# Kernel optimization log

Hardware: AMD Instinct MI355X
Metric: run time of the kernel (lower is better)

Reference implementation:

```python
import jax, jax.numpy as jnp
import numpy as np

IN_DIM, OUT_DIM = 256, 128
N_NODES, N_EDGES = 50000, 800000


def _glorot(key, shape):
    fan_in = shape[-1]
    return jax.random.normal(key, shape, dtype=jnp.float32) / jnp.sqrt(jnp.float32(fan_in))


def setup_inputs() -> dict:
    key = jax.random.key(0)
    ks = jax.random.split(key, 16)
    features1 = jax.random.normal(ks[0], (N_NODES, IN_DIM), dtype=jnp.float32)
    edge_index = jax.random.randint(ks[1], (2, N_EDGES), 0, N_NODES, dtype=jnp.int32)
    return {
        "features1": features1,
        "edge_index": edge_index,
        # encoder conv1: in->out
        "Wl_e1": _glorot(ks[2], (OUT_DIM, IN_DIM)), "bl_e1": jnp.zeros((OUT_DIM,), jnp.float32), "Wr_e1": _glorot(ks[3], (OUT_DIM, IN_DIM)),
        # encoder conv2: out->out
        "Wl_e2": _glorot(ks[4], (OUT_DIM, OUT_DIM)), "bl_e2": jnp.zeros((OUT_DIM,), jnp.float32), "Wr_e2": _glorot(ks[5], (OUT_DIM, OUT_DIM)),
        # fc: out->out
        "W_fc": _glorot(ks[6], (OUT_DIM, OUT_DIM)), "b_fc": jnp.zeros((OUT_DIM,), jnp.float32),
        # decoder conv1: out->out
        "Wl_d1": _glorot(ks[7], (OUT_DIM, OUT_DIM)), "bl_d1": jnp.zeros((OUT_DIM,), jnp.float32), "Wr_d1": _glorot(ks[8], (OUT_DIM, OUT_DIM)),
        # decoder conv2: out->in
        "Wl_d2": _glorot(ks[9], (IN_DIM, OUT_DIM)), "bl_d2": jnp.zeros((IN_DIM,), jnp.float32), "Wr_d2": _glorot(ks[10], (IN_DIM, OUT_DIM)),
    }


def _sage_conv(x, src, dst, inv_deg, Wl, bl, Wr):
    # mean aggregation of neighbor messages x[src] at destination nodes
    agg = jax.ops.segment_sum(x[src], dst, num_segments=N_NODES) * inv_deg  # [N, d_in]
    out = agg @ Wl.T + bl + x @ Wr.T  # lin_l(agg) + lin_r(x)
    # F.normalize(out, p=2, dim=-1)
    nrm = jnp.maximum(jnp.linalg.norm(out, axis=-1, keepdims=True), 1e-12)
    return out / nrm


def reference(features1, edge_index, Wl_e1, bl_e1, Wr_e1, Wl_e2, bl_e2, Wr_e2,
              W_fc, b_fc, Wl_d1, bl_d1, Wr_d1, Wl_d2, bl_d2, Wr_d2):
    src, dst = edge_index[0], edge_index[1]
    deg = jax.ops.segment_sum(jnp.ones((src.shape[0],), jnp.float32), dst, num_segments=N_NODES)
    inv_deg = (1.0 / jnp.maximum(deg, 1.0))[:, None]
    # encoder
    h = _sage_conv(features1, src, dst, inv_deg, Wl_e1, bl_e1, Wr_e1)
    x1 = _sage_conv(h, src, dst, inv_deg, Wl_e2, bl_e2, Wr_e2)
    # bottleneck linear
    x = x1 @ W_fc.T + b_fc
    # decoder
    h = _sage_conv(x, src, dst, inv_deg, Wl_d1, bl_d1, Wr_d1)
    x1_rec = _sage_conv(h, src, dst, inv_deg, Wl_d2, bl_d2, Wr_d2)
    return (x1, x1_rec)
```

## Files before the change

### kernel.cpp

```cpp
#include <hip/hip_runtime.h>
#include <hip/hip_bf16.h>
#include <math.h>

#define N_NODES 50000
#define N_EDGES 800000
#define SLOT_CAP 64

typedef short s16x8 __attribute__((ext_vector_type(8)));
typedef float f32x4 __attribute__((ext_vector_type(4)));

static __device__ __forceinline__ unsigned short f2bf(float x) {
    __hip_bfloat16 b = __float2bfloat16(x);
    return *(unsigned short*)&b;
}
static __device__ __forceinline__ float2 bfu2f2(unsigned int u) {
    __hip_bfloat162 b = *(__hip_bfloat162*)&u;
    return __bfloat1622float2(b);
}
static __device__ __forceinline__ unsigned int packbf2(float x, float y) {
    return (unsigned int)f2bf(x) | ((unsigned int)f2bf(y) << 16);
}

__global__ void k_fillslot(const int* __restrict__ src, const int* __restrict__ dst,
                           int* __restrict__ cnt, unsigned short* __restrict__ slots) {
    int e = blockIdx.x * blockDim.x + threadIdx.x;
    if (e >= N_EDGES) return;
    int d = dst[e];
    int pos = atomicAdd(&cnt[d], 1);
    if (pos < SLOT_CAP) slots[d * SLOT_CAP + pos] = (unsigned short)src[e];
}

#define FEATN (N_NODES * 256)
#define O_WL_E1 (FEATN)
#define O_WR_E1 (FEATN + 32768)
#define O_WL_E2 (FEATN + 65536)
#define O_WR_E2 (FEATN + 81920)
#define O_W_FC  (FEATN + 98304)
#define O_WL_D1 (FEATN + 114688)
#define O_WR_D1 (FEATN + 131072)
#define O_D2    (FEATN + 147456)
#define PREP_TOT (FEATN + 212992)

__global__ __launch_bounds__(256) void k_prep(const float* __restrict__ feat,
                                              const float* __restrict__ wle1, const float* __restrict__ wre1,
                                              const float* __restrict__ wle2, const float* __restrict__ wre2,
                                              const float* __restrict__ wfc,
                                              const float* __restrict__ wld1, const float* __restrict__ wrd1,
                                              const float* __restrict__ wld2, const float* __restrict__ wrd2,
                                              unsigned short* __restrict__ dstp) {
    const int tot4 = PREP_TOT / 4;
    for (int i = blockIdx.x * blockDim.x + threadIdx.x; i < tot4; i += gridDim.x * blockDim.x) {
        int e = i * 4;
        const float* s;
        int off;
        if      (e < O_WL_E1) { s = feat; off = e; }
        else if (e < O_WR_E1) { s = wle1; off = e - O_WL_E1; }
        else if (e < O_WL_E2) { s = wre1; off = e - O_WR_E1; }
        else if (e < O_WR_E2) { s = wle2; off = e - O_WL_E2; }
        else if (e < O_W_FC)  { s = wre2; off = e - O_WR_E2; }
        else if (e < O_WL_D1) { s = wfc;  off = e - O_W_FC; }
        else if (e < O_WR_D1) { s = wld1; off = e - O_WL_D1; }
        else if (e < O_D2)    { s = wrd1; off = e - O_WR_D1; }
        else {
            int rel = e - O_D2;
            int row = rel >> 8, half = (rel >> 7) & 1, col = rel & 127;
            s = half ? wrd2 : wld2;
            off = row * 128 + col;
        }
        float4 v = *(const float4*)&s[off];
        ushort4 u;
        u.x = f2bf(v.x); u.y = f2bf(v.y); u.z = f2bf(v.z); u.w = f2bf(v.w);
        *(ushort4*)&dstp[e] = u;
    }
}

template <int K>
__global__ __launch_bounds__(256) void k_gmm2(const unsigned short* __restrict__ X,
                                              const unsigned short* __restrict__ W,
                                              const float* __restrict__ bias0,
                                              const float* __restrict__ bias1,
                                              unsigned short* __restrict__ Y,
                                              int N, int Ystride) {
    constexpr int CH = K / 8;
    __shared__ unsigned short Ws[128 * K];
    const unsigned short* Wsrc = W + (size_t)blockIdx.y * 128 * K;
    for (int idx = threadIdx.x; idx < 128 * CH; idx += 256) {
        int n = idx / CH, c = idx % CH;
        uint4 v = *(const uint4*)&Wsrc[n * K + c * 8];
        int cs = c ^ (n & 15);
        *(uint4*)&Ws[n * K + cs * 8] = v;
    }
    __syncthreads();

    const int wid = threadIdx.x >> 6, lane = threadIdx.x & 63;
    const int row0 = blockIdx.x * 128 + wid * 32;
    const int lrow = lane & 15;
    const int lk8  = lane >> 4;
    f32x4 acc[2][8] = {};

    s16x8 a_cur[2];
#pragma unroll
    for (int i = 0; i < 2; i++) {
        int r = row0 + i * 16 + lrow;
        s16x8 av = {};
        if (r < N) av = *(const s16x8*)&X[(size_t)r * K + lk8 * 8];
        a_cur[i] = av;
    }

#pragma unroll
    for (int ks = 0; ks < K; ks += 32) {
        s16x8 a_nxt[2] = {};
        if (ks + 32 < K) {
#pragma unroll
            for (int i = 0; i < 2; i++) {
                int r = row0 + i * 16 + lrow;
                if (r < N) a_nxt[i] = *(const s16x8*)&X[(size_t)r * K + ks + 32 + lk8 * 8];
            }
        }
#pragma unroll
        for (int nf = 0; nf < 8; nf++) {
            int n = nf * 16 + lrow;
            int c = (ks >> 3) + lk8;
            int cs = c ^ (n & 15);
            s16x8 b = *(const s16x8*)&Ws[n * K + cs * 8];
            acc[0][nf] = __builtin_amdgcn_mfma_f32_16x16x32_bf16(a_cur[0], b, acc[0][nf], 0, 0, 0);
            acc[1][nf] = __builtin_amdgcn_mfma_f32_16x16x32_bf16(a_cur[1], b, acc[1][nf], 0, 0, 0);
        }
        a_cur[0] = a_nxt[0];
        a_cur[1] = a_nxt[1];
    }

    const float* bias = (blockIdx.y == 0) ? bias0 : bias1;
    const int ccol = lane & 15, crow0 = (lane >> 4) * 4;
    const int ycol0 = blockIdx.y * 128;
#pragma unroll
    for (int nf = 0; nf < 8; nf++) {
        int lcol = nf * 16 + ccol;
        float bv = bias ? bias[lcol] : 0.0f;
#pragma unroll
        for (int i = 0; i < 2; i++) {
#pragma unroll
            for (int j = 0; j < 4; j++) {
                int grow = row0 + i * 16 + crow0 + j;
                if (grow < N) Y[(size_t)grow * Ystride + ycol0 + lcol] = f2bf(acc[i][nf][j] + bv);
            }
        }
    }
}

__global__ __launch_bounds__(256) void k_gmmn(const unsigned short* __restrict__ X,
                                              const unsigned short* __restrict__ W,
                                              const float* __restrict__ bias,
                                              float* __restrict__ OUT, int N) {
    __shared__ unsigned short Ws[128 * 256];
    const int wid = threadIdx.x >> 6, lane = threadIdx.x & 63;
    const int row0 = blockIdx.x * 128 + wid * 32;
    const int lrow = lane & 15;
    const int lk8  = lane >> 4;
    const int ccol = lane & 15, crow0 = (lane >> 4) * 4;
    f32x4 acc[2][2][8] = {};

#pragma unroll
    for (int half = 0; half < 2; half++) {
        __syncthreads();
        const unsigned short* Wsrc = W + (size_t)half * 128 * 256;
        for (int idx = threadIdx.x; idx < 128 * 32; idx += 256) {
            int n = idx / 32, c = idx % 32;
            uint4 v = *(const uint4*)&Wsrc[n * 256 + c * 8];
            int cs = c ^ (n & 15);
            *(uint4*)&Ws[n * 256 + cs * 8] = v;
        }
        __syncthreads();

        s16x8 a_cur[2];
#pragma unroll
        for (int i = 0; i < 2; i++) {
            int r = row0 + i * 16 + lrow;
            s16x8 av = {};
            if (r < N) av = *(const s16x8*)&X[(size_t)r * 256 + lk8 * 8];
            a_cur[i] = av;
        }
#pragma unroll
        for (int ks = 0; ks < 256; ks += 32) {
            s16x8 a_nxt[2] = {};
            if (ks + 32 < 256) {
#pragma unroll
                for (int i = 0; i < 2; i++) {
                    int r = row0 + i * 16 + lrow;
                    if (r < N) a_nxt[i] = *(const s16x8*)&X[(size_t)r * 256 + ks + 32 + lk8 * 8];
                }
            }
#pragma unroll
            for (int nf = 0; nf < 8; nf++) {
                int n = nf * 16 + lrow;
                int c = (ks >> 3) + lk8;
                int cs = c ^ (n & 15);
                s16x8 b = *(const s16x8*)&Ws[n * 256 + cs * 8];
                acc[half][0][nf] = __builtin_amdgcn_mfma_f32_16x16x32_bf16(a_cur[0], b, acc[half][0][nf], 0, 0, 0);
                acc[half][1][nf] = __builtin_amdgcn_mfma_f32_16x16x32_bf16(a_cur[1], b, acc[half][1][nf], 0, 0, 0);
            }
            a_cur[0] = a_nxt[0];
            a_cur[1] = a_nxt[1];
        }
    }

#pragma unroll
    for (int half = 0; half < 2; half++)
#pragma unroll
        for (int nf = 0; nf < 8; nf++) {
            float bv = bias[half * 128 + nf * 16 + ccol];
#pragma unroll
            for (int i = 0; i < 2; i++)
#pragma unroll
                for (int j = 0; j < 4; j++) acc[half][i][nf][j] += bv;
        }
    float rs[2][4];
#pragma unroll
    for (int i = 0; i < 2; i++)
#pragma unroll
        for (int j = 0; j < 4; j++) {
            float ss = 0.0f;
#pragma unroll
            for (int half = 0; half < 2; half++)
#pragma unroll
                for (int nf = 0; nf < 8; nf++) ss += acc[half][i][nf][j] * acc[half][i][nf][j];
            ss += __shfl_xor(ss, 1); ss += __shfl_xor(ss, 2);
            ss += __shfl_xor(ss, 4); ss += __shfl_xor(ss, 8);
            rs[i][j] = 1.0f / fmaxf(sqrtf(ss), 1e-12f);
        }
#pragma unroll
    for (int i = 0; i < 2; i++)
#pragma unroll
        for (int j = 0; j < 4; j++) {
            int grow = row0 + i * 16 + crow0 + j;
            if (grow < N) {
                float r = rs[i][j];
#pragma unroll
                for (int half = 0; half < 2; half++)
#pragma unroll
                    for (int nf = 0; nf < 8; nf++)
                        OUT[(size_t)grow * 256 + half * 128 + nf * 16 + ccol] = acc[half][i][nf][j] * r;
            }
        }
}

template <bool WRITE_F32>
__global__ __launch_bounds__(256) void k_aggfin4(const uint4* __restrict__ TP,
                                                 const unsigned short* __restrict__ slots,
                                                 const int* __restrict__ cnt,
                                                 float* __restrict__ OUTF,
                                                 uint4* __restrict__ OUTB,
                                                 int ostride4, int ooff4) {
    const int wave = (blockIdx.x * blockDim.x + threadIdx.x) >> 6;
    const int lane = threadIdx.x & 63;
    if (wave >= N_NODES) return;
    const int q = lane & 15, sub = lane >> 4;
    int deg = cnt[wave];
    deg = min(deg, SLOT_CAP);
    const int base = wave * SLOT_CAP;
    float acc[8] = {};
    int i = sub * 4;
    for (; i + 3 < deg; i += 16) {
        ushort4 nb = *(const ushort4*)&slots[base + i];
        uint4 v0 = TP[(size_t)nb.x * 32 + q];
        uint4 v1 = TP[(size_t)nb.y * 32 + q];
        uint4 v2 = TP[(size_t)nb.z * 32 + q];
        uint4 v3 = TP[(size_t)nb.w * 32 + q];
        float2 a0 = bfu2f2(v0.x), a1 = bfu2f2(v0.y), a2 = bfu2f2(v0.z), a3 = bfu2f2(v0.w);
        float2 b0 = bfu2f2(v1.x), b1 = bfu2f2(v1.y), b2 = bfu2f2(v1.z), b3 = bfu2f2(v1.w);
        float2 c0 = bfu2f2(v2.x), c1 = bfu2f2(v2.y), c2 = bfu2f2(v2.z), c3 = bfu2f2(v2.w);
        float2 d0 = bfu2f2(v3.x), d1 = bfu2f2(v3.y), d2 = bfu2f2(v3.z), d3 = bfu2f2(v3.w);
        acc[0] += (a0.x + b0.x) + (c0.x + d0.x); acc[1] += (a0.y + b0.y) + (c0.y + d0.y);
        acc[2] += (a1.x + b1.x) + (c1.x + d1.x); acc[3] += (a1.y + b1.y) + (c1.y + d1.y);
        acc[4] += (a2.x + b2.x) + (c2.x + d2.x); acc[5] += (a2.y + b2.y) + (c2.y + d2.y);
        acc[6] += (a3.x + b3.x) + (c3.x + d3.x); acc[7] += (a3.y + b3.y) + (c3.y + d3.y);
    }
    const int r0 = deg & ~3;
    if (sub == ((r0 >> 2) & 3)) {
        for (int j = r0; j < deg; j++) {
            uint4 v = TP[(size_t)slots[base + j] * 32 + q];
            float2 a0 = bfu2f2(v.x), a1 = bfu2f2(v.y), a2 = bfu2f2(v.z), a3 = bfu2f2(v.w);
            acc[0] += a0.x; acc[1] += a0.y; acc[2] += a1.x; acc[3] += a1.y;
            acc[4] += a2.x; acc[5] += a2.y; acc[6] += a3.x; acc[7] += a3.y;
        }
    }
#pragma unroll
    for (int k = 0; k < 8; k++) {
        acc[k] += __shfl_xor(acc[k], 16);
        acc[k] += __shfl_xor(acc[k], 32);
    }
    const float inv = 1.0f / fmaxf((float)deg, 1.0f);
    uint4 pv = TP[(size_t)wave * 32 + 16 + q];
    float2 p0 = bfu2f2(pv.x), p1 = bfu2f2(pv.y), p2 = bfu2f2(pv.z), p3 = bfu2f2(pv.w);
    float o[8];
    o[0] = p0.x + inv * acc[0]; o[1] = p0.y + inv * acc[1];
    o[2] = p1.x + inv * acc[2]; o[3] = p1.y + inv * acc[3];
    o[4] = p2.x + inv * acc[4]; o[5] = p2.y + inv * acc[5];
    o[6] = p3.x + inv * acc[6]; o[7] = p3.y + inv * acc[7];
    float ss = 0.0f;
#pragma unroll
    for (int k = 0; k < 8; k++) ss += o[k] * o[k];
    ss += __shfl_xor(ss, 1); ss += __shfl_xor(ss, 2);
    ss += __shfl_xor(ss, 4); ss += __shfl_xor(ss, 8);
    float r = 1.0f / fmaxf(sqrtf(ss), 1e-12f);
#pragma unroll
    for (int k = 0; k < 8; k++) o[k] *= r;
    if (lane < 16) {
        if constexpr (WRITE_F32) {
            ((float4*)OUTF)[(size_t)wave * 32 + q * 2]     = make_float4(o[0], o[1], o[2], o[3]);
            ((float4*)OUTF)[(size_t)wave * 32 + q * 2 + 1] = make_float4(o[4], o[5], o[6], o[7]);
        }
        uint4 u;
        u.x = packbf2(o[0], o[1]); u.y = packbf2(o[2], o[3]);
        u.z = packbf2(o[4], o[5]); u.w = packbf2(o[6], o[7]);
        OUTB[(size_t)wave * ostride4 + ooff4 + q] = u;
    }
}

__global__ __launch_bounds__(256) void k_agg4(const uint4* __restrict__ IN,
                                              const unsigned short* __restrict__ slots,
                                              const int* __restrict__ cnt,
                                              uint4* __restrict__ OUT,
                                              int istride4, int ioff4, int ostride4, int ooff4) {
    const int wave = (blockIdx.x * blockDim.x + threadIdx.x) >> 6;
    const int lane = threadIdx.x & 63;
    if (wave >= N_NODES) return;
    const int q = lane & 15, sub = lane >> 4;
    int deg = cnt[wave];
    deg = min(deg, SLOT_CAP);
    const int base = wave * SLOT_CAP;
    float acc[8] = {};
    int i = sub * 4;
    for (; i + 3 < deg; i += 16) {
        ushort4 nb = *(const ushort4*)&slots[base + i];
        uint4 v0 = IN[(size_t)nb.x * istride4 + ioff4 + q];
        uint4 v1 = IN[(size_t)nb.y * istride4 + ioff4 + q];
        uint4 v2 = IN[(size_t)nb.z * istride4 + ioff4 + q];
        uint4 v3 = IN[(size_t)nb.w * istride4 + ioff4 + q];
        float2 a0 = bfu2f2(v0.x), a1 = bfu2f2(v0.y), a2 = bfu2f2(v0.z), a3 = bfu2f2(v0.w);
        float2 b0 = bfu2f2(v1.x), b1 = bfu2f2(v1.y), b2 = bfu2f2(v1.z), b3 = bfu2f2(v1.w);
        float2 c0 = bfu2f2(v2.x), c1 = bfu2f2(v2.y), c2 = bfu2f2(v2.z), c3 = bfu2f2(v2.w);
        float2 d0 = bfu2f2(v3.x), d1 = bfu2f2(v3.y), d2 = bfu2f2(v3.z), d3 = bfu2f2(v3.w);
        acc[0] += (a0.x + b0.x) + (c0.x + d0.x); acc[1] += (a0.y + b0.y) + (c0.y + d0.y);
        acc[2] += (a1.x + b1.x) + (c1.x + d1.x); acc[3] += (a1.y + b1.y) + (c1.y + d1.y);
        acc[4] += (a2.x + b2.x) + (c2.x + d2.x); acc[5] += (a2.y + b2.y) + (c2.y + d2.y);
        acc[6] += (a3.x + b3.x) + (c3.x + d3.x); acc[7] += (a3.y + b3.y) + (c3.y + d3.y);
    }
    const int r0 = deg & ~3;
    if (sub == ((r0 >> 2) & 3)) {
        for (int j = r0; j < deg; j++) {
            uint4 v = IN[(size_t)slots[base + j] * istride4 + ioff4 + q];
            float2 a0 = bfu2f2(v.x), a1 = bfu2f2(v.y), a2 = bfu2f2(v.z), a3 = bfu2f2(v.w);
            acc[0] += a0.x; acc[1] += a0.y; acc[2] += a1.x; acc[3] += a1.y;
            acc[4] += a2.x; acc[5] += a2.y; acc[6] += a3.x; acc[7] += a3.y;
        }
    }
#pragma unroll
    for (int k = 0; k < 8; k++) {
        acc[k] += __shfl_xor(acc[k], 16);
        acc[k] += __shfl_xor(acc[k], 32);
    }
    const float inv = 1.0f / fmaxf((float)deg, 1.0f);
    if (lane < 16) {
        uint4 u;
        u.x = packbf2(inv * acc[0], inv * acc[1]);
        u.y = packbf2(inv * acc[2], inv * acc[3]);
        u.z = packbf2(inv * acc[4], inv * acc[5]);
        u.w = packbf2(inv * acc[6], inv * acc[7]);
        OUT[(size_t)wave * ostride4 + ooff4 + q] = u;
    }
}

extern "C" void kernel_launch(void* const* d_in, const int* in_sizes, int n_in,
                              void* d_out, int out_size, void* d_ws, size_t ws_size,
                              hipStream_t stream) {
    const float* feat  = (const float*)d_in[0];
    const int*   ei    = (const int*)d_in[1];
    const int*   src   = ei;
    const int*   dst   = ei + N_EDGES;
    const float* Wl_e1 = (const float*)d_in[2];
    const float* bl_e1 = (const float*)d_in[3];
    const float* Wr_e1 = (const float*)d_in[4];
    const float* Wl_e2 = (const float*)d_in[5];
    const float* bl_e2 = (const float*)d_in[6];
    const float* Wr_e2 = (const float*)d_in[7];
    const float* W_fc  = (const float*)d_in[8];
    const float* b_fc  = (const float*)d_in[9];
    const float* Wl_d1 = (const float*)d_in[10];
    const float* bl_d1 = (const float*)d_in[11];
    const float* Wr_d1 = (const float*)d_in[12];
    const float* Wl_d2 = (const float*)d_in[13];
    const float* bl_d2 = (const float*)d_in[14];
    const float* Wr_d2 = (const float*)d_in[15];

    char* w = (char*)d_ws;
    auto alloc = [&](size_t bytes) -> void* {
        void* p = (void*)w;
        w += (bytes + 255) & ~(size_t)255;
        return p;
    };
    int* cnt   = (int*)alloc((size_t)N_NODES * 4);
    unsigned short* slots = (unsigned short*)alloc((size_t)N_NODES * SLOT_CAP * 2);
    unsigned short* bfpool = (unsigned short*)alloc((size_t)PREP_TOT * 2);
    unsigned short* TP   = (unsigned short*)alloc((size_t)N_NODES * 256 * 2);
    unsigned short* hb   = (unsigned short*)alloc((size_t)N_NODES * 128 * 2);
    unsigned short* x1b  = (unsigned short*)alloc((size_t)N_NODES * 128 * 2);
    unsigned short* X2   = (unsigned short*)alloc((size_t)N_NODES * 256 * 2);

    unsigned short* featb = bfpool;
    float* x1     = (float*)d_out;
    float* x1_rec = (float*)d_out + (size_t)N_NODES * 128;

    hipMemsetAsync(cnt, 0, (size_t)N_NODES * 4, stream);

    const int EB = (N_EDGES + 255) / 256;
    k_prep<<<2048, 256, 0, stream>>>(feat, Wl_e1, Wr_e1, Wl_e2, Wr_e2, W_fc, Wl_d1, Wr_d1, Wl_d2, Wr_d2, bfpool);
    k_fillslot<<<EB, 256, 0, stream>>>(src, dst, cnt, slots);

    const int NB128 = (N_NODES + 127) / 128;
    const int WPB   = (N_NODES * 64 + 255) / 256;

    k_gmm2<256><<<dim3(NB128, 2), 256, 0, stream>>>(featb, bfpool + O_WL_E1, nullptr, bl_e1, TP, N_NODES, 256);
    k_aggfin4<false><<<WPB, 256, 0, stream>>>((const uint4*)TP, slots, cnt, nullptr, (uint4*)hb, 16, 0);
    k_gmm2<128><<<dim3(NB128, 2), 256, 0, stream>>>(hb, bfpool + O_WL_E2, nullptr, bl_e2, TP, N_NODES, 256);
    k_aggfin4<true><<<WPB, 256, 0, stream>>>((const uint4*)TP, slots, cnt, x1, (uint4*)x1b, 16, 0);
    k_gmm2<128><<<dim3(NB128, 1), 256, 0, stream>>>(x1b, bfpool + O_W_FC, b_fc, nullptr, hb, N_NODES, 128);
    k_gmm2<128><<<dim3(NB128, 2), 256, 0, stream>>>(hb, bfpool + O_WL_D1, nullptr, bl_d1, TP, N_NODES, 256);
    k_aggfin4<false><<<WPB, 256, 0, stream>>>((const uint4*)TP, slots, cnt, nullptr, (uint4*)X2, 32, 16);
    k_agg4<<<WPB, 256, 0, stream>>>((const uint4*)X2, slots, cnt, (uint4*)X2, 32, 16, 32, 0);
    k_gmmn<<<NB128, 256, 0, stream>>>(X2, bfpool + O_D2, bl_d2, x1_rec, N_NODES);
}
```

Before: 351.8 us.

## Fuse bf16 prep conversion and edge slot filling into one kernel

Merges the fp32-to-bf16 conversion kernel and the edge slot-filling kernel into a single launch, with separate block ranges doing each job so they run concurrently. The fill part now partitions edges by destination modulo 8 across block groups, with each group scanning all edges but handling only its own partition. This removes one kernel launch and lets the memory-bound conversion overlap the atomic-heavy fill. In exchange, each fill group rereads the whole dst array, and the slot order inside each node can change.

Measured after the change: 341.8 us. 2.8% less time.

```diff
diff --git a/kernel.cpp b/kernel.cpp
--- a/kernel.cpp
+++ b/kernel.cpp
@@ -19,15 +19,6 @@
 }
 static __device__ __forceinline__ unsigned int packbf2(float x, float y) {
     return (unsigned int)f2bf(x) | ((unsigned int)f2bf(y) << 16);
-}
-
-__global__ void k_fillslot(const int* __restrict__ src, const int* __restrict__ dst,
-                           int* __restrict__ cnt, unsigned short* __restrict__ slots) {
-    int e = blockIdx.x * blockDim.x + threadIdx.x;
-    if (e >= N_EDGES) return;
-    int d = dst[e];
-    int pos = atomicAdd(&cnt[d], 1);
-    if (pos < SLOT_CAP) slots[d * SLOT_CAP + pos] = (unsigned short)src[e];
 }
 
 #define FEATN (N_NODES * 256)
@@ -41,36 +32,53 @@
 #define O_D2    (FEATN + 147456)
 #define PREP_TOT (FEATN + 212992)
 
-__global__ __launch_bounds__(256) void k_prep(const float* __restrict__ feat,
-                                              const float* __restrict__ wle1, const float* __restrict__ wre1,
-                                              const float* __restrict__ wle2, const float* __restrict__ wre2,
-                                              const float* __restrict__ wfc,
-                                              const float* __restrict__ wld1, const float* __restrict__ wrd1,
-                                              const float* __restrict__ wld2, const float* __restrict__ wrd2,
-                                              unsigned short* __restrict__ dstp) {
-    const int tot4 = PREP_TOT / 4;
-    for (int i = blockIdx.x * blockDim.x + threadIdx.x; i < tot4; i += gridDim.x * blockDim.x) {
-        int e = i * 4;
-        const float* s;
-        int off;
-        if      (e < O_WL_E1) { s = feat; off = e; }
-        else if (e < O_WR_E1) { s = wle1; off = e - O_WL_E1; }
-        else if (e < O_WL_E2) { s = wre1; off = e - O_WR_E1; }
-        else if (e < O_WR_E2) { s = wle2; off = e - O_WL_E2; }
-        else if (e < O_W_FC)  { s = wre2; off = e - O_WR_E2; }
-        else if (e < O_WL_D1) { s = wfc;  off = e - O_W_FC; }
-        else if (e < O_WR_D1) { s = wld1; off = e - O_WL_D1; }
-        else if (e < O_D2)    { s = wrd1; off = e - O_WR_D1; }
-        else {
-            int rel = e - O_D2;
-            int row = rel >> 8, half = (rel >> 7) & 1, col = rel & 127;
-            s = half ? wrd2 : wld2;
-            off = row * 128 + col;
-        }
-        float4 v = *(const float4*)&s[off];
-        ushort4 u;
-        u.x = f2bf(v.x); u.y = f2bf(v.y); u.z = f2bf(v.z); u.w = f2bf(v.w);
-        *(ushort4*)&dstp[e] = u;
+#define PREP_BLOCKS 2048
+#define FILL_BLOCKS 1024
+
+__global__ __launch_bounds__(256) void k_pf(const float* __restrict__ feat,
+                                            const float* __restrict__ wle1, const float* __restrict__ wre1,
+                                            const float* __restrict__ wle2, const float* __restrict__ wre2,
+                                            const float* __restrict__ wfc,
+                                            const float* __restrict__ wld1, const float* __restrict__ wrd1,
+                                            const float* __restrict__ wld2, const float* __restrict__ wrd2,
+                                            unsigned short* __restrict__ dstp,
+                                            const int* __restrict__ esrc, const int* __restrict__ edst,
+                                            int* __restrict__ cnt, unsigned short* __restrict__ slots) {
+    if (blockIdx.x < PREP_BLOCKS) {
+        const int tot4 = PREP_TOT / 4;
+        for (int i = blockIdx.x * blockDim.x + threadIdx.x; i < tot4; i += PREP_BLOCKS * 256) {
+            int e = i * 4;
+            const float* s;
+            int off;
+            if      (e < O_WL_E1) { s = feat; off = e; }
+            else if (e < O_WR_E1) { s = wle1; off = e - O_WL_E1; }
+            else if (e < O_WL_E2) { s = wre1; off = e - O_WR_E1; }
+            else if (e < O_WR_E2) { s = wle2; off = e - O_WL_E2; }
+            else if (e < O_W_FC)  { s = wre2; off = e - O_WR_E2; }
+            else if (e < O_WL_D1) { s = wfc;  off = e - O_W_FC; }
+            else if (e < O_WR_D1) { s = wld1; off = e - O_WL_D1; }
+            else if (e < O_D2)    { s = wrd1; off = e - O_WR_D1; }
+            else {
+                int rel = e - O_D2;
+                int row = rel >> 8, half = (rel >> 7) & 1, col = rel & 127;
+                s = half ? wrd2 : wld2;
+                off = row * 128 + col;
+            }
+            float4 v = *(const float4*)&s[off];
+            ushort4 u;
+            u.x = f2bf(v.x); u.y = f2bf(v.y); u.z = f2bf(v.z); u.w = f2bf(v.w);
+            *(ushort4*)&dstp[e] = u;
+        }
+    } else {
+        const int fb = blockIdx.x - PREP_BLOCKS;
+        const int p = fb & 7;
+        const int stride = (FILL_BLOCKS >> 3) * 256;
+        for (int e = (fb >> 3) * 256 + threadIdx.x; e < N_EDGES; e += stride) {
+            int d = edst[e];
+            if ((d & 7) != p) continue;
+            int pos = atomicAdd(&cnt[d], 1);
+            if (pos < SLOT_CAP) slots[d * SLOT_CAP + pos] = (unsigned short)esrc[e];
+        }
     }
 }
 
@@ -413,9 +421,9 @@
 
     hipMemsetAsync(cnt, 0, (size_t)N_NODES * 4, stream);
 
-    const int EB = (N_EDGES + 255) / 256;
-    k_prep<<<2048, 256, 0, stream>>>(feat, Wl_e1, Wr_e1, Wl_e2, Wr_e2, W_fc, Wl_d1, Wr_d1, Wl_d2, Wr_d2, bfpool);
-    k_fillslot<<<EB, 256, 0, stream>>>(src, dst, cnt, slots);
+    k_pf<<<PREP_BLOCKS + FILL_BLOCKS, 256, 0, stream>>>(
+        feat, Wl_e1, Wr_e1, Wl_e2, Wr_e2, W_fc, Wl_d1, Wr_d1, Wl_d2, Wr_d2, bfpool,
+        src, dst, cnt, slots);
 
     const int NB128 = (N_NODES + 127) / 128;
     const int WPB   = (N_NODES * 64 + 255) / 256;
```

## Fold fc layer into decoder conv1 weights and fuse slot fill into first GEMM

Applied to the files above, without the earlier changes.

Precomputes the products Wl_d1·W_fc and Wr_d1·W_fc plus the matching bias terms in a small compose kernel, so the separate bottleneck linear GEMM over all nodes is removed. The edge slot-filling work now runs as extra blocks inside the first encoder GEMM launch so it can overlap with matrix work, and slots are stored as int instead of ushort. This drops a full-size GEMM pass and a kernel launch but doubles slot storage and read traffic, and composing the weights in fp32 before the bf16 cast changes rounding slightly.

After: 328.6 us. 1.07x faster.

```diff
diff --git a/kernel.cpp b/kernel.cpp
--- a/kernel.cpp
+++ b/kernel.cpp
@@ -5,6 +5,8 @@
 #define N_NODES 50000
 #define N_EDGES 800000
 #define SLOT_CAP 64
+#define NB128 391
+#define FILLB 1024
 
 typedef short s16x8 __attribute__((ext_vector_type(8)));
 typedef float f32x4 __attribute__((ext_vector_type(4)));
@@ -19,15 +21,6 @@
 }
 static __device__ __forceinline__ unsigned int packbf2(float x, float y) {
     return (unsigned int)f2bf(x) | ((unsigned int)f2bf(y) << 16);
-}
-
-__global__ void k_fillslot(const int* __restrict__ src, const int* __restrict__ dst,
-                           int* __restrict__ cnt, unsigned short* __restrict__ slots) {
-    int e = blockIdx.x * blockDim.x + threadIdx.x;
-    if (e >= N_EDGES) return;
-    int d = dst[e];
-    int pos = atomicAdd(&cnt[d], 1);
-    if (pos < SLOT_CAP) slots[d * SLOT_CAP + pos] = (unsigned short)src[e];
 }
 
 #define FEATN (N_NODES * 256)
@@ -35,17 +28,14 @@
 #define O_WR_E1 (FEATN + 32768)
 #define O_WL_E2 (FEATN + 65536)
 #define O_WR_E2 (FEATN + 81920)
-#define O_W_FC  (FEATN + 98304)
-#define O_WL_D1 (FEATN + 114688)
-#define O_WR_D1 (FEATN + 131072)
-#define O_D2    (FEATN + 147456)
-#define PREP_TOT (FEATN + 212992)
+#define O_D2    (FEATN + 98304)
+#define PREP_TOT (FEATN + 163840)
+#define O_WD1C  (FEATN + 163840)
+#define POOL_TOT (FEATN + 196608)
 
 __global__ __launch_bounds__(256) void k_prep(const float* __restrict__ feat,
                                               const float* __restrict__ wle1, const float* __restrict__ wre1,
                                               const float* __restrict__ wle2, const float* __restrict__ wre2,
-                                              const float* __restrict__ wfc,
-                                              const float* __restrict__ wld1, const float* __restrict__ wrd1,
                                               const float* __restrict__ wld2, const float* __restrict__ wrd2,
                                               unsigned short* __restrict__ dstp) {
     const int tot4 = PREP_TOT / 4;
@@ -57,10 +47,7 @@
         else if (e < O_WR_E1) { s = wle1; off = e - O_WL_E1; }
         else if (e < O_WL_E2) { s = wre1; off = e - O_WR_E1; }
         else if (e < O_WR_E2) { s = wle2; off = e - O_WL_E2; }
-        else if (e < O_W_FC)  { s = wre2; off = e - O_WR_E2; }
-        else if (e < O_WL_D1) { s = wfc;  off = e - O_W_FC; }
-        else if (e < O_WR_D1) { s = wld1; off = e - O_WL_D1; }
-        else if (e < O_D2)    { s = wrd1; off = e - O_WR_D1; }
+        else if (e < O_D2)    { s = wre2; off = e - O_WR_E2; }
         else {
             int rel = e - O_D2;
             int row = rel >> 8, half = (rel >> 7) & 1, col = rel & 127;
@@ -71,6 +58,103 @@
         ushort4 u;
         u.x = f2bf(v.x); u.y = f2bf(v.y); u.z = f2bf(v.z); u.w = f2bf(v.w);
         *(ushort4*)&dstp[e] = u;
+    }
+}
+
+__global__ __launch_bounds__(128) void k_compose(const float* __restrict__ wld1,
+                                                 const float* __restrict__ wrd1,
+                                                 const float* __restrict__ wfc,
+                                                 const float* __restrict__ bfc,
+                                                 const float* __restrict__ bld1,
+                                                 unsigned short* __restrict__ outw,
+                                                 float* __restrict__ bT, float* __restrict__ bP) {
+    const float* WX = blockIdx.y ? wrd1 : wld1;
+    if (blockIdx.x < 128) {
+        int r = blockIdx.x, c = threadIdx.x;
+        float acc = 0.0f;
+        for (int j = 0; j < 128; j++) acc += WX[r * 128 + j] * wfc[j * 128 + c];
+        outw[blockIdx.y * 16384 + r * 128 + c] = f2bf(acc);
+    } else {
+        int t = threadIdx.x;
+        float acc = 0.0f;
+        for (int j = 0; j < 128; j++) acc += WX[t * 128 + j] * bfc[j];
+        if (blockIdx.y == 0) bT[t] = acc;
+        else                 bP[t] = acc + bld1[t];
+    }
+}
+
+template <int K>
+static __device__ __forceinline__ void gemm_body(int bxm, int by,
+                                                 const unsigned short* __restrict__ X,
+                                                 const unsigned short* __restrict__ W,
+                                                 const float* __restrict__ bias0,
+                                                 const float* __restrict__ bias1,
+                                                 unsigned short* __restrict__ Y,
+                                                 int N, int Ystride) {
+    constexpr int CH = K / 8;
+    __shared__ unsigned short Ws[128 * K];
+    const unsigned short* Wsrc = W + (size_t)by * 128 * K;
+    for (int idx = threadIdx.x; idx < 128 * CH; idx += 256) {
+        int n = idx / CH, c = idx % CH;
+        uint4 v = *(const uint4*)&Wsrc[n * K + c * 8];
+        int cs = c ^ (n & 15);
+        *(uint4*)&Ws[n * K + cs * 8] = v;
+    }
+    __syncthreads();
+
+    const int wid = threadIdx.x >> 6, lane = threadIdx.x & 63;
+    const int row0 = bxm * 128 + wid * 32;
+    const int lrow = lane & 15;
+    const int lk8  = lane >> 4;
+    f32x4 acc[2][8] = {};
+
+    s16x8 a_cur[2];
+#pragma unroll
+    for (int i = 0; i < 2; i++) {
+        int r = row0 + i * 16 + lrow;
+        s16x8 av = {};
+        if (r < N) av = *(const s16x8*)&X[(size_t)r * K + lk8 * 8];
+        a_cur[i] = av;
+    }
+
+#pragma unroll
+    for (int ks = 0; ks < K; ks += 32) {
+        s16x8 a_nxt[2] = {};
+        if (ks + 32 < K) {
+#pragma unroll
+            for (int i = 0; i < 2; i++) {
+                int r = row0 + i * 16 + lrow;
+                if (r < N) a_nxt[i] = *(const s16x8*)&X[(size_t)r * K + ks + 32 + lk8 * 8];
+            }
+        }
+#pragma unroll
+        for (int nf = 0; nf < 8; nf++) {
+            int n = nf * 16 + lrow;
+            int c = (ks >> 3) + lk8;
+            int cs = c ^ (n & 15);
+            s16x8 b = *(const s16x8*)&Ws[n * K + cs * 8];
+            acc[0][nf] = __builtin_amdgcn_mfma_f32_16x16x32_bf16(a_cur[0], b, acc[0][nf], 0, 0, 0);
+            acc[1][nf] = __builtin_amdgcn_mfma_f32_16x16x32_bf16(a_cur[1], b, acc[1][nf], 0, 0, 0);
+        }
+        a_cur[0] = a_nxt[0];
+        a_cur[1] = a_nxt[1];
+    }
+
+    const float* bias = (by == 0) ? bias0 : bias1;
+    const int ccol = lane & 15, crow0 = (lane >> 4) * 4;
+    const int ycol0 = by * 128;
+#pragma unroll
+    for (int nf = 0; nf < 8; nf++) {
+        int lcol = nf * 16 + ccol;
+        float bv = bias ? bias[lcol] : 0.0f;
+#pragma unroll
+        for (int i = 0; i < 2; i++) {
+#pragma unroll
+            for (int j = 0; j < 4; j++) {
+                int grow = row0 + i * 16 + crow0 + j;
+                if (grow < N) Y[(size_t)grow * Ystride + ycol0 + lcol] = f2bf(acc[i][nf][j] + bv);
+            }
+        }
     }
 }
 
@@ -81,69 +165,25 @@
                                               const float* __restrict__ bias1,
                                               unsigned short* __restrict__ Y,
                                               int N, int Ystride) {
-    constexpr int CH = K / 8;
-    __shared__ unsigned short Ws[128 * K];
-    const unsigned short* Wsrc = W + (size_t)blockIdx.y * 128 * K;
-    for (int idx = threadIdx.x; idx < 128 * CH; idx += 256) {
-        int n = idx / CH, c = idx % CH;
-        uint4 v = *(const uint4*)&Wsrc[n * K + c * 8];
-        int cs = c ^ (n & 15);
-        *(uint4*)&Ws[n * K + cs * 8] = v;
-    }
-    __syncthreads();
-
-    const int wid = threadIdx.x >> 6, lane = threadIdx.x & 63;
-    const int row0 = blockIdx.x * 128 + wid * 32;
-    const int lrow = lane & 15;
-    const int lk8  = lane >> 4;
-    f32x4 acc[2][8] = {};
-
-    s16x8 a_cur[2];
-#pragma unroll
-    for (int i = 0; i < 2; i++) {
-        int r = row0 + i * 16 + lrow;
-        s16x8 av = {};
-        if (r < N) av = *(const s16x8*)&X[(size_t)r * K + lk8 * 8];
-        a_cur[i] = av;
-    }
-
-#pragma unroll
-    for (int ks = 0; ks < K; ks += 32) {
-        s16x8 a_nxt[2] = {};
-        if (ks + 32 < K) {
-#pragma unroll
-            for (int i = 0; i < 2; i++) {
-                int r = row0 + i * 16 + lrow;
-                if (r < N) a_nxt[i] = *(const s16x8*)&X[(size_t)r * K + ks + 32 + lk8 * 8];
-            }
-        }
-#pragma unroll
-        for (int nf = 0; nf < 8; nf++) {
-            int n = nf * 16 + lrow;
-            int c = (ks >> 3) + lk8;
-            int cs = c ^ (n & 15);
-            s16x8 b = *(const s16x8*)&Ws[n * K + cs * 8];
-            acc[0][nf] = __builtin_amdgcn_mfma_f32_16x16x32_bf16(a_cur[0], b, acc[0][nf], 0, 0, 0);
-            acc[1][nf] = __builtin_amdgcn_mfma_f32_16x16x32_bf16(a_cur[1], b, acc[1][nf], 0, 0, 0);
-        }
-        a_cur[0] = a_nxt[0];
-        a_cur[1] = a_nxt[1];
-    }
-
-    const float* bias = (blockIdx.y == 0) ? bias0 : bias1;
-    const int ccol = lane & 15, crow0 = (lane >> 4) * 4;
-    const int ycol0 = blockIdx.y * 128;
-#pragma unroll
-    for (int nf = 0; nf < 8; nf++) {
-        int lcol = nf * 16 + ccol;
-        float bv = bias ? bias[lcol] : 0.0f;
-#pragma unroll
-        for (int i = 0; i < 2; i++) {
-#pragma unroll
-            for (int j = 0; j < 4; j++) {
-                int grow = row0 + i * 16 + crow0 + j;
-                if (grow < N) Y[(size_t)grow * Ystride + ycol0 + lcol] = f2bf(acc[i][nf][j] + bv);
-            }
+    gemm_body<K>(blockIdx.x, blockIdx.y, X, W, bias0, bias1, Y, N, Ystride);
+}
+
+__global__ __launch_bounds__(256) void k_g1f(const unsigned short* __restrict__ X,
+                                             const unsigned short* __restrict__ W,
+                                             const float* __restrict__ bias1,
+                                             unsigned short* __restrict__ Y,
+                                             const int* __restrict__ esrc,
+                                             const int* __restrict__ edst,
+                                             int* __restrict__ cnt,
+                                             int* __restrict__ slots) {
+    if (blockIdx.x < 2 * NB128) {
+        gemm_body<256>(blockIdx.x >> 1, blockIdx.x & 1, X, W, nullptr, bias1, Y, N_NODES, 256);
+    } else {
+        const int fb = blockIdx.x - 2 * NB128;
+        for (int e = fb * 256 + threadIdx.x; e < N_EDGES; e += FILLB * 256) {
+            int d = edst[e];
+            int pos = atomicAdd(&cnt[d], 1);
+            if (pos < SLOT_CAP) slots[d * SLOT_CAP + pos] = esrc[e];
         }
     }
 }
@@ -246,7 +286,7 @@
 
 template <bool WRITE_F32>
 __global__ __launch_bounds__(256) void k_aggfin4(const uint4* __restrict__ TP,
-                                                 const unsigned short* __restrict__ slots,
+                                                 const int* __restrict__ slots,
                                                  const int* __restrict__ cnt,
                                                  float* __restrict__ OUTF,
                                                  uint4* __restrict__ OUTB,
@@ -261,7 +301,7 @@
     float acc[8] = {};
     int i = sub * 4;
     for (; i + 3 < deg; i += 16) {
-        ushort4 nb = *(const ushort4*)&slots[base + i];
+        int4 nb = *(const int4*)&slots[base + i];
         uint4 v0 = TP[(size_t)nb.x * 32 + q];
         uint4 v1 = TP[(size_t)nb.y * 32 + q];
         uint4 v2 = TP[(size_t)nb.z * 32 + q];
@@ -318,7 +358,7 @@
 }
 
 __global__ __launch_bounds__(256) void k_agg4(const uint4* __restrict__ IN,
-                                              const unsigned short* __restrict__ slots,
+                                              const int* __restrict__ slots,
                                               const int* __restrict__ cnt,
                                               uint4* __restrict__ OUT,
                                               int istride4, int ioff4, int ostride4, int ooff4) {
@@ -332,7 +372,7 @@
     float acc[8] = {};
     int i = sub * 4;
     for (; i + 3 < deg; i += 16) {
-        ushort4 nb = *(const ushort4*)&slots[base + i];
+        int4 nb = *(const int4*)&slots[base + i];
         uint4 v0 = IN[(size_t)nb.x * istride4 + ioff4 + q];
         uint4 v1 = IN[(size_t)nb.y * istride4 + ioff4 + q];
         uint4 v2 = IN[(size_t)nb.z * istride4 + ioff4 + q];
@@ -400,12 +440,14 @@
         return p;
     };
     int* cnt   = (int*)alloc((size_t)N_NODES * 4);
-    unsigned short* slots = (unsigned short*)alloc((size_t)N_NODES * SLOT_CAP * 2);
-    unsigned short* bfpool = (unsigned short*)alloc((size_t)PREP_TOT * 2);
+    int* slots = (int*)alloc((size_t)N_NODES * SLOT_CAP * 4);
+    unsigned short* bfpool = (unsigned short*)alloc((size_t)POOL_TOT * 2);
     unsigned short* TP   = (unsigned short*)alloc((size_t)N_NODES * 256 * 2);
     unsigned short* hb   = (unsigned short*)alloc((size_t)N_NODES * 128 * 2);
     unsigned short* x1b  = (unsigned short*)alloc((size_t)N_NODES * 128 * 2);
     unsigned short* X2   = (unsigned short*)alloc((size_t)N_NODES * 256 * 2);
+    float* bT = (float*)alloc(128 * 4);
+    float* bP = (float*)alloc(128 * 4);
 
     unsigned short* featb = bfpool;
     float* x1     = (float*)d_out;
@@ -413,19 +455,18 @@
 
     hipMemsetAsync(cnt, 0, (size_t)N_NODES * 4, stream);
 
-    const int EB = (N_EDGES + 255) / 256;
-    k_prep<<<2048, 256, 0, stream>>>(feat, Wl_e1, Wr_e1, Wl_e2, Wr_e2, W_fc, Wl_d1, Wr_d1, Wl_d2, Wr_d2, bfpool);
-    k_fillslot<<<EB, 256, 0, stream>>>(src, dst, cnt, slots);
-
-    const int NB128 = (N_NODES + 127) / 128;
-    const int WPB   = (N_NODES * 64 + 255) / 256;
-
-    k_gmm2<256><<<dim3(NB128, 2), 256, 0, stream>>>(featb, bfpool + O_WL_E1, nullptr, bl_e1, TP, N_NODES, 256);
+    k_compose<<<dim3(129, 2), 128, 0, stream>>>(Wl_d1, Wr_d1, W_fc, b_fc, bl_d1,
+                                                bfpool + O_WD1C, bT, bP);
+    k_prep<<<2048, 256, 0, stream>>>(feat, Wl_e1, Wr_e1, Wl_e2, Wr_e2, Wl_d2, Wr_d2, bfpool);
+
+    const int WPB = (N_NODES * 64 + 255) / 256;
+
+    k_g1f<<<2 * NB128 + FILLB, 256, 0, stream>>>(featb, bfpool + O_WL_E1, bl_e1, TP,
+                                                 src, dst, cnt, slots);
     k_aggfin4<false><<<WPB, 256, 0, stream>>>((const uint4*)TP, slots, cnt, nullptr, (uint4*)hb, 16, 0);
     k_gmm2<128><<<dim3(NB128, 2), 256, 0, stream>>>(hb, bfpool + O_WL_E2, nullptr, bl_e2, TP, N_NODES, 256);
     k_aggfin4<true><<<WPB, 256, 0, stream>>>((const uint4*)TP, slots, cnt, x1, (uint4*)x1b, 16, 0);
-    k_gmm2<128><<<dim3(NB128, 1), 256, 0, stream>>>(x1b, bfpool + O_W_FC, b_fc, nullptr, hb, N_NODES, 128);
-    k_gmm2<128><<<dim3(NB128, 2), 256, 0, stream>>>(hb, bfpool + O_WL_D1, nullptr, bl_d1, TP, N_NODES, 256);
+    k_gmm2<128><<<dim3(NB128, 2), 256, 0, stream>>>(x1b, bfpool + O_WD1C, bT, bP, TP, N_NODES, 256);
     k_aggfin4<false><<<WPB, 256, 0, stream>>>((const uint4*)TP, slots, cnt, nullptr, (uint4*)X2, 32, 16);
     k_agg4<<<WPB, 256, 0, stream>>>((const uint4*)X2, slots, cnt, (uint4*)X2, 32, 16, 32, 0);
     k_gmmn<<<NB128, 256, 0, stream>>>(X2, bfpool + O_D2, bl_d2, x1_rec, N_NODES);
```
